# Performance work log

Hardware: AMD Instinct MI355X
Metric: run time of the kernel (lower is better)

Reference implementation:

```python
import jax, jax.numpy as jnp
import numpy as np

HIDDEN = 256
B, SQ, SKV = 8, 2048, 2048
SCALE = float(np.sqrt(HIDDEN / 2.0))  # module uses sqrt(hidden_dim/2)


def setup_inputs() -> dict:
    key = jax.random.key(0)
    ks = jax.random.split(key, 9)
    s = 1.0 / np.sqrt(HIDDEN)
    return {
        "query": jax.random.normal(ks[0], (B, SQ, HIDDEN), jnp.float32),
        "key": jax.random.normal(ks[1], (B, SKV, HIDDEN), jnp.float32),
        "value": jax.random.normal(ks[2], (B, SKV, HIDDEN), jnp.float32),
        "Wq": jax.random.uniform(ks[3], (HIDDEN, HIDDEN), jnp.float32, -s, s),
        "bq": jax.random.uniform(ks[4], (HIDDEN,), jnp.float32, -s, s),
        "Wk": jax.random.uniform(ks[5], (HIDDEN, HIDDEN), jnp.float32, -s, s),
        "bk": jax.random.uniform(ks[6], (HIDDEN,), jnp.float32, -s, s),
        "Wv": jax.random.uniform(ks[7], (HIDDEN, HIDDEN), jnp.float32, -s, s),
        "bv": jax.random.uniform(ks[8], (HIDDEN,), jnp.float32, -s, s),
    }


def reference(query, key, value, Wq, bq, Wk, bk, Wv, bv):
    # Linear projections (torch Linear: x @ W.T + b)
    Q = jnp.einsum('bsd,ed->bse', query, Wq) + bq  # [B,SQ,H]
    K = jnp.einsum('bsd,ed->bse', key, Wk) + bk    # [B,SKV,H]
    V = jnp.einsum('bsd,ed->bse', value, Wv) + bv  # [B,SKV,H]
    scores = jnp.einsum('bqd,bkd->bqk', Q, K) / SCALE  # [B,SQ,SKV]
    weights = jax.nn.softmax(scores, axis=-1)
    return jnp.einsum('bqk,bkd->bqd', weights, V)  # [B,SQ,H]
```

## Files before the change

kernel.cpp:

```cpp
#include <hip/hip_runtime.h>

#define HID 256
#define NB 8
#define SQL 2048
#define SKV 2048
#define SPLIT 4
#define KPB (SKV / SPLIT)
#define KVB 32
#define NT (KPB / KVB)
#define NROW (NB * SQL)

typedef __attribute__((ext_vector_type(8))) short bf16x8;
typedef __attribute__((ext_vector_type(4))) float f32x4;

static __device__ __forceinline__ unsigned short f2bf(float x) {
  union { float f; unsigned int u; } v; v.f = x;
  unsigned int r = v.u + 0x7FFFu + ((v.u >> 16) & 1u);
  return (unsigned short)(r >> 16);
}

__global__ void wconv_kernel(const float* __restrict__ Wq, const float* __restrict__ Wk,
                             const float* __restrict__ Wv, unsigned short* __restrict__ out) {
  int i = blockIdx.x * blockDim.x + threadIdx.x;
  if (i >= 3 * HID * HID) return;
  const float* src = (i < HID * HID) ? Wq : (i < 2 * HID * HID ? Wk : Wv);
  out[i] = f2bf(src[i & (HID * HID - 1)]);
}

__global__ __launch_bounds__(512, 4) void proj_kernel(
    const float* __restrict__ query, const float* __restrict__ key, const float* __restrict__ value,
    const unsigned short* __restrict__ Wb,
    const float* __restrict__ bq, const float* __restrict__ bk, const float* __restrict__ bv,
    unsigned short* __restrict__ Qb, unsigned short* __restrict__ KFo, unsigned short* __restrict__ VFo) {
  __shared__ __align__(16) char wl[65536];
  int tid = threadIdx.x;
  int wave = tid >> 6, lane = tid & 63, lr = lane & 15, lg = lane >> 4;
  int blk = blockIdx.x;
  int mat = blk >> 8;
  int rem = blk & 255;
  int b = rem >> 5;
  int rt = (rem >> 1) & 15;
  int et = rem & 1;

  const float* X = (mat == 0) ? query : (mat == 1 ? key : value);
  const float* bias = (mat == 0) ? bq : (mat == 1 ? bk : bv);
  const char* Wsrc = (const char*)(Wb + mat * HID * HID + et * 128 * HID);

#pragma unroll
  for (int i = 0; i < 8; i++) {
    int c = i * 512 + tid;
    int e = c >> 5;
    int glo = e * 512 + (((c & 31) ^ (e & 7)) << 4);
    __builtin_amdgcn_global_load_lds(
        (const __attribute__((address_space(1))) unsigned int*)(Wsrc + glo),
        (__attribute__((address_space(3))) unsigned int*)(wl + c * 16), 16, 0, 0);
  }

  int row_a = rt * 128 + wave * 16 + lr;
  const float* xrow = X + ((size_t)(b * SQL + row_a)) * HID;
  bf16x8 af[8];
#pragma unroll
  for (int s = 0; s < 8; s++) {
    const float4* p = (const float4*)(xrow + s * 32 + lg * 8);
    float4 x0 = p[0], x1 = p[1];
    bf16x8 a;
    a[0] = (short)f2bf(x0.x); a[1] = (short)f2bf(x0.y); a[2] = (short)f2bf(x0.z); a[3] = (short)f2bf(x0.w);
    a[4] = (short)f2bf(x1.x); a[5] = (short)f2bf(x1.y); a[6] = (short)f2bf(x1.z); a[7] = (short)f2bf(x1.w);
    af[s] = a;
  }
  __syncthreads();

  int row_c = rt * 128 + wave * 16 + lg * 4;
#pragma unroll
  for (int eo = 0; eo < 8; eo++) {
    f32x4 acc = (f32x4){0.f, 0.f, 0.f, 0.f};
    int eL = eo * 16 + lr;
#pragma unroll
    for (int sl = 0; sl < 8; sl++) {
      bf16x8 bfr = *(const bf16x8*)(wl + eL * 512 + (((sl * 4 + lg) ^ (eL & 7)) << 4));
      acc = __builtin_amdgcn_mfma_f32_16x16x32_bf16(af[sl], bfr, acc, 0, 0, 0);
    }
    int e = et * 128 + eo * 16 + lr;
    float bv_ = bias[e];
    if (mat == 0) {
      unsigned short* dst = Qb + (size_t)(b * SQL) * HID;
#pragma unroll
      for (int i = 0; i < 4; i++)
        dst[(size_t)(row_c + i) * HID + e] = f2bf(acc[i] + bv_);
    } else if (mat == 1) {
      int s = e >> 5, gg = (e >> 3) & 3, j = e & 7;
#pragma unroll
      for (int i = 0; i < 4; i++) {
        int row = row_c + i;
        int k5 = row & 31;
        int half = (k5 >> 2) & 1;
        int lidx = (((k5 >> 3) << 2) | (k5 & 3)) + 16 * gg;
        size_t frag = (size_t)(b * 1024 + (row >> 5) * 16 + half * 8 + s);
        KFo[frag * 512 + lidx * 8 + j] = f2bf(acc[i] + bv_);
      }
    } else {
      int dt = e >> 4, l15 = e & 15;
#pragma unroll
      for (int i = 0; i < 4; i++) {
        int row = row_c + i;
        int gg = (row >> 3) & 3, j = row & 7;
        size_t frag = (size_t)(b * 1024 + (row >> 5) * 16 + dt);
        VFo[frag * 512 + (l15 + 16 * gg) * 8 + j] = f2bf(acc[i] + bv_);
      }
    }
  }
}

__global__ __launch_bounds__(256, 2) void attn_kernel(
    const unsigned short* __restrict__ Qb, const char* __restrict__ KF,
    const char* __restrict__ VF, unsigned short* __restrict__ Op,
    float* __restrict__ Ml) {
  extern __shared__ char smem[];
  int tid = threadIdx.x;
  int wave = tid >> 6, lane = tid & 63, l15 = lane & 15, g = lane >> 4;
  int L = (blockIdx.x & 7) * 64 + (blockIdx.x >> 3);
  int b = L >> 6, sp = (L >> 4) & 3, qt = L & 15;
  int q0 = qt * 128 + wave * 32;

  const char* Ks0 = KF + ((size_t)(b * 64 + sp * 16)) * 16384;
  const char* Vs0 = VF + ((size_t)(b * 64 + sp * 16)) * 16384;

  auto stage = [&](int t, char* kb, char* vb) {
    const char* Ks = Ks0 + (size_t)t * 16384;
    const char* Vs = Vs0 + (size_t)t * 16384;
#pragma unroll
    for (int i = 0; i < 4; i++)
      __builtin_amdgcn_global_load_lds(
          (const __attribute__((address_space(1))) unsigned int*)(Ks + i * 4096 + tid * 16),
          (__attribute__((address_space(3))) unsigned int*)(kb + i * 4096 + tid * 16),
          16, 0, 0);
#pragma unroll
    for (int i = 0; i < 4; i++)
      __builtin_amdgcn_global_load_lds(
          (const __attribute__((address_space(1))) unsigned int*)(Vs + i * 4096 + tid * 16),
          (__attribute__((address_space(3))) unsigned int*)(vb + i * 4096 + tid * 16),
          16, 0, 0);
  };

  bf16x8 qfa[8], qfb[8];
  {
    const unsigned short* qa = Qb + ((size_t)(b * SQL + q0 + l15)) * HID + g * 8;
    const unsigned short* qb2 = qa + 16 * HID;
#pragma unroll
    for (int s = 0; s < 8; s++) {
      qfa[s] = *(const bf16x8*)(qa + s * 32);
      qfb[s] = *(const bf16x8*)(qb2 + s * 32);
    }
  }

  f32x4 acc0[16], acc1[16];
#pragma unroll
  for (int dt = 0; dt < 16; dt++) {
    acc0[dt] = (f32x4){0.f, 0.f, 0.f, 0.f};
    acc1[dt] = (f32x4){0.f, 0.f, 0.f, 0.f};
  }
  float m0 = -1e30f, l0 = 0.f, m1 = -1e30f, l1 = 0.f;
  const float kC = 1.44269504088896341f / 11.3137084989847604f;

  auto step = [&](const char* kb, const char* vb) {
    const char* kbl = kb + lane * 16;
    const char* vbl = vb + lane * 16;
    f32x4 p0a = (f32x4){0.f,0.f,0.f,0.f}, p1a = (f32x4){0.f,0.f,0.f,0.f};
    f32x4 p0b = (f32x4){0.f,0.f,0.f,0.f}, p1b = (f32x4){0.f,0.f,0.f,0.f};
#pragma unroll
    for (int s = 0; s < 8; s++) {
      bf16x8 kf0 = *(const bf16x8*)(kbl + s * 1024);
      bf16x8 kf1 = *(const bf16x8*)(kbl + (8 + s) * 1024);
      p0a = __builtin_amdgcn_mfma_f32_16x16x32_bf16(kf0, qfa[s], p0a, 0, 0, 0);
      p1a = __builtin_amdgcn_mfma_f32_16x16x32_bf16(kf1, qfa[s], p1a, 0, 0, 0);
      p0b = __builtin_amdgcn_mfma_f32_16x16x32_bf16(kf0, qfb[s], p0b, 0, 0, 0);
      p1b = __builtin_amdgcn_mfma_f32_16x16x32_bf16(kf1, qfb[s], p1b, 0, 0, 0);
    }

    float ta = fmaxf(fmaxf(fmaxf(p0a[0], p0a[1]), fmaxf(p0a[2], p0a[3])),
                     fmaxf(fmaxf(p1a[0], p1a[1]), fmaxf(p1a[2], p1a[3])));
    float tb = fmaxf(fmaxf(fmaxf(p0b[0], p0b[1]), fmaxf(p0b[2], p0b[3])),
                     fmaxf(fmaxf(p1b[0], p1b[1]), fmaxf(p1b[2], p1b[3])));
    ta = fmaxf(ta, __shfl_xor(ta, 16, 64)); tb = fmaxf(tb, __shfl_xor(tb, 16, 64));
    ta = fmaxf(ta, __shfl_xor(ta, 32, 64)); tb = fmaxf(tb, __shfl_xor(tb, 32, 64));
    float msa = ta * kC, msb = tb * kC;
    if (!__all(msa <= m0 + 8.0f)) {
      float mn = fmaxf(m0, msa);
      float al = exp2f(m0 - mn);
      l0 *= al; m0 = mn;
#pragma unroll
      for (int dt = 0; dt < 16; dt++)
#pragma unroll
        for (int i = 0; i < 4; i++) acc0[dt][i] *= al;
    }
    if (!__all(msb <= m1 + 8.0f)) {
      float mn = fmaxf(m1, msb);
      float al = exp2f(m1 - mn);
      l1 *= al; m1 = mn;
#pragma unroll
      for (int dt = 0; dt < 16; dt++)
#pragma unroll
        for (int i = 0; i < 4; i++) acc1[dt][i] *= al;
    }
#pragma unroll
    for (int i = 0; i < 4; i++) {
      p0a[i] = exp2f(fmaf(p0a[i], kC, -m0)); p1a[i] = exp2f(fmaf(p1a[i], kC, -m0));
      p0b[i] = exp2f(fmaf(p0b[i], kC, -m1)); p1b[i] = exp2f(fmaf(p1b[i], kC, -m1));
    }
    float sa = (p0a[0] + p0a[1]) + (p0a[2] + p0a[3]) + (p1a[0] + p1a[1]) + (p1a[2] + p1a[3]);
    float sb = (p0b[0] + p0b[1]) + (p0b[2] + p0b[3]) + (p1b[0] + p1b[1]) + (p1b[2] + p1b[3]);
    sa += __shfl_xor(sa, 16, 64); sb += __shfl_xor(sb, 16, 64);
    sa += __shfl_xor(sa, 32, 64); sb += __shfl_xor(sb, 32, 64);
    l0 += sa; l1 += sb;

    unsigned wa0, wa1, wa2, wa3, wb0, wb1, wb2, wb3;
    asm("v_cvt_pk_bf16_f32 %0, %1, %2" : "=v"(wa0) : "v"(p0a[0]), "v"(p0a[1]));
    asm("v_cvt_pk_bf16_f32 %0, %1, %2" : "=v"(wa1) : "v"(p0a[2]), "v"(p0a[3]));
    asm("v_cvt_pk_bf16_f32 %0, %1, %2" : "=v"(wa2) : "v"(p1a[0]), "v"(p1a[1]));
    asm("v_cvt_pk_bf16_f32 %0, %1, %2" : "=v"(wa3) : "v"(p1a[2]), "v"(p1a[3]));
    asm("v_cvt_pk_bf16_f32 %0, %1, %2" : "=v"(wb0) : "v"(p0b[0]), "v"(p0b[1]));
    asm("v_cvt_pk_bf16_f32 %0, %1, %2" : "=v"(wb1) : "v"(p0b[2]), "v"(p0b[3]));
    asm("v_cvt_pk_bf16_f32 %0, %1, %2" : "=v"(wb2) : "v"(p1b[0]), "v"(p1b[1]));
    asm("v_cvt_pk_bf16_f32 %0, %1, %2" : "=v"(wb3) : "v"(p1b[2]), "v"(p1b[3]));
    union { unsigned u[4]; bf16x8 v; } pa, pb;
    pa.u[0] = wa0; pa.u[1] = wa1; pa.u[2] = wa2; pa.u[3] = wa3;
    pb.u[0] = wb0; pb.u[1] = wb1; pb.u[2] = wb2; pb.u[3] = wb3;

#pragma unroll
    for (int dt = 0; dt < 16; dt++) {
      bf16x8 vf = *(const bf16x8*)(vbl + dt * 1024);
      acc0[dt] = __builtin_amdgcn_mfma_f32_16x16x32_bf16(vf, pa.v, acc0[dt], 0, 0, 0);
      acc1[dt] = __builtin_amdgcn_mfma_f32_16x16x32_bf16(vf, pb.v, acc1[dt], 0, 0, 0);
    }
  };

  stage(0, smem, smem + 32768);
  __syncthreads();
  for (int t = 0; t < NT; t++) {
    char* kb = smem + (t & 1) * 16384;
    char* vb = smem + 32768 + (t & 1) * 16384;
    if (t + 1 < NT)
      stage(t + 1, smem + ((t + 1) & 1) * 16384, smem + 32768 + ((t + 1) & 1) * 16384);
    step(kb, vb);
    __syncthreads();
  }

  size_t rowA = (size_t)b * SQL + q0 + l15;
  size_t rowB = rowA + 16;
  if (g == 0) {
    float2 mlA; mlA.x = m0; mlA.y = l0;
    float2 mlB; mlB.x = m1; mlB.y = l1;
    *(float2*)(Ml + ((size_t)sp * NROW + rowA) * 2) = mlA;
    *(float2*)(Ml + ((size_t)sp * NROW + rowB) * 2) = mlB;
  }
  float li0 = 1.0f / l0, li1 = 1.0f / l1;
  unsigned short* oA = Op + ((size_t)sp * NROW + rowA) * HID;
  unsigned short* oB = Op + ((size_t)sp * NROW + rowB) * HID;
#pragma unroll
  for (int dt = 0; dt < 16; dt++) {
    ushort4 v0, v1;
    union { _Float16 hf; unsigned short u; } c;
    c.hf = (_Float16)(acc0[dt][0] * li0); v0.x = c.u;
    c.hf = (_Float16)(acc0[dt][1] * li0); v0.y = c.u;
    c.hf = (_Float16)(acc0[dt][2] * li0); v0.z = c.u;
    c.hf = (_Float16)(acc0[dt][3] * li0); v0.w = c.u;
    c.hf = (_Float16)(acc1[dt][0] * li1); v1.x = c.u;
    c.hf = (_Float16)(acc1[dt][1] * li1); v1.y = c.u;
    c.hf = (_Float16)(acc1[dt][2] * li1); v1.z = c.u;
    c.hf = (_Float16)(acc1[dt][3] * li1); v1.w = c.u;
    *(ushort4*)(oA + dt * 16 + g * 4) = v0;
    *(ushort4*)(oB + dt * 16 + g * 4) = v1;
  }
}

__global__ __launch_bounds__(256) void comb_kernel(const unsigned short* __restrict__ Op,
                                                   const float* __restrict__ Ml,
                                                   float* __restrict__ out) {
  int idx = blockIdx.x * 256 + threadIdx.x;
  int row = idx >> 6;
  int d0 = (idx & 63) << 2;
  float mv[SPLIT], lv[SPLIT];
#pragma unroll
  for (int s = 0; s < SPLIT; s++) {
    float2 ml = *(const float2*)(Ml + ((size_t)s * NROW + row) * 2);
    mv[s] = ml.x; lv[s] = ml.y;
  }
  float M = mv[0];
#pragma unroll
  for (int s = 1; s < SPLIT; s++) M = fmaxf(M, mv[s]);
  float W = 0.f, w[SPLIT];
#pragma unroll
  for (int s = 0; s < SPLIT; s++) { w[s] = lv[s] * exp2f(mv[s] - M); W += w[s]; }
  float wi = 1.0f / W;
  float o0 = 0.f, o1 = 0.f, o2 = 0.f, o3 = 0.f;
#pragma unroll
  for (int s = 0; s < SPLIT; s++) {
    ushort4 u = *(const ushort4*)(Op + ((size_t)s * NROW + row) * HID + d0);
    union { unsigned short us; _Float16 hf; } c0, c1, c2, c3;
    c0.us = u.x; c1.us = u.y; c2.us = u.z; c3.us = u.w;
    o0 += w[s] * (float)c0.hf; o1 += w[s] * (float)c1.hf;
    o2 += w[s] * (float)c2.hf; o3 += w[s] * (float)c3.hf;
  }
  float4 res; res.x = o0 * wi; res.y = o1 * wi; res.z = o2 * wi; res.w = o3 * wi;
  *(float4*)(out + (size_t)row * HID + d0) = res;
}

extern "C" void kernel_launch(void* const* d_in, const int* in_sizes, int n_in,
                              void* d_out, int out_size, void* d_ws, size_t ws_size,
                              hipStream_t stream) {
  const float* query = (const float*)d_in[0];
  const float* key   = (const float*)d_in[1];
  const float* value = (const float*)d_in[2];
  const float* Wq = (const float*)d_in[3];
  const float* bq = (const float*)d_in[4];
  const float* Wk = (const float*)d_in[5];
  const float* bk = (const float*)d_in[6];
  const float* Wv = (const float*)d_in[7];
  const float* bv = (const float*)d_in[8];

  char* ws = (char*)d_ws;
  unsigned short* Wb  = (unsigned short*)ws;
  unsigned short* Qb  = (unsigned short*)(ws + 393216);
  unsigned short* KF  = Qb + (size_t)NB * SQL * HID;
  unsigned short* VF  = KF + (size_t)NB * SKV * HID;
  unsigned short* Op  = VF + (size_t)NB * HID * SKV;
  float* Ml = (float*)(Op + (size_t)SPLIT * NROW * HID);

  hipLaunchKernelGGL(wconv_kernel, dim3(768), dim3(256), 0, stream, Wq, Wk, Wv, Wb);
  hipLaunchKernelGGL(proj_kernel, dim3(768), dim3(512), 0, stream,
                     query, key, value, Wb, bq, bk, bv, Qb, KF, VF);
  hipLaunchKernelGGL(attn_kernel, dim3(512), dim3(256), 65536, stream,
                     Qb, (const char*)KF, (const char*)VF, Op, Ml);
  hipLaunchKernelGGL(comb_kernel, dim3(4096), dim3(256), 0, stream, Op, Ml, (float*)d_out);
}
```

Baseline: 92.24 us.

## Reuse input fragments across both output halves and add separate K fragment transpose kernel

The projection kernel now covers both 128-column halves of the output in one block, loading each weight half into LDS in turn. This halves the grid and avoids converting the same input rows to bf16 twice. K is written row-major into scratch space that aliases the partial-output buffer, then reordered into the fragment layout by a new small transpose kernel, which replaces scattered 2-byte stores with 16-byte copies. V stores become packed ushort4 writes. In attention, the per-tile cross-lane shuffle reduction of the row sum is moved to after the loop, at the cost of one extra kernel launch and an extra round trip of K through memory.

```diff
diff --git a/kernel.cpp b/kernel.cpp
--- a/kernel.cpp
+++ b/kernel.cpp
@@ -27,34 +27,22 @@
   out[i] = f2bf(src[i & (HID * HID - 1)]);
 }
 
-__global__ __launch_bounds__(512, 4) void proj_kernel(
+__global__ __launch_bounds__(512, 2) void proj_kernel(
     const float* __restrict__ query, const float* __restrict__ key, const float* __restrict__ value,
     const unsigned short* __restrict__ Wb,
     const float* __restrict__ bq, const float* __restrict__ bk, const float* __restrict__ bv,
-    unsigned short* __restrict__ Qb, unsigned short* __restrict__ KFo, unsigned short* __restrict__ VFo) {
+    unsigned short* __restrict__ Qb, unsigned short* __restrict__ Kr, unsigned short* __restrict__ VFo) {
   __shared__ __align__(16) char wl[65536];
   int tid = threadIdx.x;
   int wave = tid >> 6, lane = tid & 63, lr = lane & 15, lg = lane >> 4;
   int blk = blockIdx.x;
-  int mat = blk >> 8;
-  int rem = blk & 255;
-  int b = rem >> 5;
-  int rt = (rem >> 1) & 15;
-  int et = rem & 1;
+  int mat = blk >> 7;
+  int rem = blk & 127;
+  int b = rem >> 4;
+  int rt = rem & 15;
 
   const float* X = (mat == 0) ? query : (mat == 1 ? key : value);
   const float* bias = (mat == 0) ? bq : (mat == 1 ? bk : bv);
-  const char* Wsrc = (const char*)(Wb + mat * HID * HID + et * 128 * HID);
-
-#pragma unroll
-  for (int i = 0; i < 8; i++) {
-    int c = i * 512 + tid;
-    int e = c >> 5;
-    int glo = e * 512 + (((c & 31) ^ (e & 7)) << 4);
-    __builtin_amdgcn_global_load_lds(
-        (const __attribute__((address_space(1))) unsigned int*)(Wsrc + glo),
-        (__attribute__((address_space(3))) unsigned int*)(wl + c * 16), 16, 0, 0);
-  }
 
   int row_a = rt * 128 + wave * 16 + lr;
   const float* xrow = X + ((size_t)(b * SQL + row_a)) * HID;
@@ -68,47 +56,60 @@
     a[4] = (short)f2bf(x1.x); a[5] = (short)f2bf(x1.y); a[6] = (short)f2bf(x1.z); a[7] = (short)f2bf(x1.w);
     af[s] = a;
   }
-  __syncthreads();
 
   int row_c = rt * 128 + wave * 16 + lg * 4;
-#pragma unroll
-  for (int eo = 0; eo < 8; eo++) {
-    f32x4 acc = (f32x4){0.f, 0.f, 0.f, 0.f};
-    int eL = eo * 16 + lr;
-#pragma unroll
-    for (int sl = 0; sl < 8; sl++) {
-      bf16x8 bfr = *(const bf16x8*)(wl + eL * 512 + (((sl * 4 + lg) ^ (eL & 7)) << 4));
-      acc = __builtin_amdgcn_mfma_f32_16x16x32_bf16(af[sl], bfr, acc, 0, 0, 0);
-    }
-    int e = et * 128 + eo * 16 + lr;
-    float bv_ = bias[e];
-    if (mat == 0) {
-      unsigned short* dst = Qb + (size_t)(b * SQL) * HID;
-#pragma unroll
-      for (int i = 0; i < 4; i++)
-        dst[(size_t)(row_c + i) * HID + e] = f2bf(acc[i] + bv_);
-    } else if (mat == 1) {
-      int s = e >> 5, gg = (e >> 3) & 3, j = e & 7;
-#pragma unroll
-      for (int i = 0; i < 4; i++) {
-        int row = row_c + i;
-        int k5 = row & 31;
-        int half = (k5 >> 2) & 1;
-        int lidx = (((k5 >> 3) << 2) | (k5 & 3)) + 16 * gg;
-        size_t frag = (size_t)(b * 1024 + (row >> 5) * 16 + half * 8 + s);
-        KFo[frag * 512 + lidx * 8 + j] = f2bf(acc[i] + bv_);
+  for (int et = 0; et < 2; ++et) {
+    if (et) __syncthreads();
+    const char* Wsrc = (const char*)(Wb + mat * HID * HID + et * 128 * HID);
+#pragma unroll
+    for (int i = 0; i < 8; i++) {
+      int c = i * 512 + tid;
+      int e = c >> 5;
+      int glo = e * 512 + (((c & 31) ^ (e & 7)) << 4);
+      __builtin_amdgcn_global_load_lds(
+          (const __attribute__((address_space(1))) unsigned int*)(Wsrc + glo),
+          (__attribute__((address_space(3))) unsigned int*)(wl + c * 16), 16, 0, 0);
+    }
+    __syncthreads();
+
+#pragma unroll
+    for (int eo = 0; eo < 8; eo++) {
+      f32x4 acc = (f32x4){0.f, 0.f, 0.f, 0.f};
+      int eL = eo * 16 + lr;
+#pragma unroll
+      for (int sl = 0; sl < 8; sl++) {
+        bf16x8 bfr = *(const bf16x8*)(wl + eL * 512 + (((sl * 4 + lg) ^ (eL & 7)) << 4));
+        acc = __builtin_amdgcn_mfma_f32_16x16x32_bf16(af[sl], bfr, acc, 0, 0, 0);
       }
-    } else {
-      int dt = e >> 4, l15 = e & 15;
-#pragma unroll
-      for (int i = 0; i < 4; i++) {
-        int row = row_c + i;
-        int gg = (row >> 3) & 3, j = row & 7;
-        size_t frag = (size_t)(b * 1024 + (row >> 5) * 16 + dt);
-        VFo[frag * 512 + (l15 + 16 * gg) * 8 + j] = f2bf(acc[i] + bv_);
+      int e = et * 128 + eo * 16 + lr;
+      float bv_ = bias[e];
+      if (mat < 2) {
+        unsigned short* dst = (mat == 0 ? Qb : Kr) + (size_t)(b * SQL) * HID;
+#pragma unroll
+        for (int i = 0; i < 4; i++)
+          dst[(size_t)(row_c + i) * HID + e] = f2bf(acc[i] + bv_);
+      } else {
+        int jb = 4 * ((row_c >> 4) & 1);
+        size_t frag = (size_t)b * 1024 + (size_t)(row_c >> 5) * 16 + (et * 8 + eo);
+        ushort4 v;
+        v.x = f2bf(acc[0] + bv_); v.y = f2bf(acc[1] + bv_);
+        v.z = f2bf(acc[2] + bv_); v.w = f2bf(acc[3] + bv_);
+        *(ushort4*)(VFo + frag * 512 + (lr + 16 * lg) * 8 + jb) = v;
       }
     }
   }
+}
+
+__global__ __launch_bounds__(256) void ktr_kernel(const unsigned short* __restrict__ Kr,
+                                                  unsigned short* __restrict__ KFo) {
+  int o = blockIdx.x * 256 + threadIdx.x;
+  int cidx = o & 63, frag = o >> 6;
+  int b = frag >> 10, r = frag & 1023;
+  int tile = r >> 4, half = (r >> 3) & 1, s = r & 7;
+  int l15 = cidx & 15, g = cidx >> 4;
+  int ky = tile * 32 + half * 16 + l15;
+  *(float4*)(KFo + (size_t)frag * 512 + cidx * 8) =
+      *(const float4*)(Kr + ((size_t)b * SKV + ky) * HID + s * 32 + g * 8);
 }
 
 __global__ __launch_bounds__(256, 2) void attn_kernel(
@@ -207,11 +208,8 @@
       p0a[i] = exp2f(fmaf(p0a[i], kC, -m0)); p1a[i] = exp2f(fmaf(p1a[i], kC, -m0));
       p0b[i] = exp2f(fmaf(p0b[i], kC, -m1)); p1b[i] = exp2f(fmaf(p1b[i], kC, -m1));
     }
-    float sa = (p0a[0] + p0a[1]) + (p0a[2] + p0a[3]) + (p1a[0] + p1a[1]) + (p1a[2] + p1a[3]);
-    float sb = (p0b[0] + p0b[1]) + (p0b[2] + p0b[3]) + (p1b[0] + p1b[1]) + (p1b[2] + p1b[3]);
-    sa += __shfl_xor(sa, 16, 64); sb += __shfl_xor(sb, 16, 64);
-    sa += __shfl_xor(sa, 32, 64); sb += __shfl_xor(sb, 32, 64);
-    l0 += sa; l1 += sb;
+    l0 += (p0a[0] + p0a[1]) + (p0a[2] + p0a[3]) + (p1a[0] + p1a[1]) + (p1a[2] + p1a[3]);
+    l1 += (p0b[0] + p0b[1]) + (p0b[2] + p0b[3]) + (p1b[0] + p1b[1]) + (p1b[2] + p1b[3]);
 
     unsigned wa0, wa1, wa2, wa3, wb0, wb1, wb2, wb3;
     asm("v_cvt_pk_bf16_f32 %0, %1, %2" : "=v"(wa0) : "v"(p0a[0]), "v"(p0a[1]));
@@ -244,6 +242,9 @@
     step(kb, vb);
     __syncthreads();
   }
+
+  l0 += __shfl_xor(l0, 16, 64); l0 += __shfl_xor(l0, 32, 64);
+  l1 += __shfl_xor(l1, 16, 64); l1 += __shfl_xor(l1, 32, 64);
 
   size_t rowA = (size_t)b * SQL + q0 + l15;
   size_t rowB = rowA + 16;
@@ -325,10 +326,12 @@
   unsigned short* VF  = KF + (size_t)NB * SKV * HID;
   unsigned short* Op  = VF + (size_t)NB * HID * SKV;
   float* Ml = (float*)(Op + (size_t)SPLIT * NROW * HID);
+  unsigned short* Kr = Op;
 
   hipLaunchKernelGGL(wconv_kernel, dim3(768), dim3(256), 0, stream, Wq, Wk, Wv, Wb);
-  hipLaunchKernelGGL(proj_kernel, dim3(768), dim3(512), 0, stream,
-                     query, key, value, Wb, bq, bk, bv, Qb, KF, VF);
+  hipLaunchKernelGGL(proj_kernel, dim3(384), dim3(512), 0, stream,
+                     query, key, value, Wb, bq, bk, bv, Qb, Kr, VF);
+  hipLaunchKernelGGL(ktr_kernel, dim3(2048), dim3(256), 0, stream, Kr, KF);
   hipLaunchKernelGGL(attn_kernel, dim3(512), dim3(256), 65536, stream,
                      Qb, (const char*)KF, (const char*)VF, Op, Ml);
   hipLaunchKernelGGL(comb_kernel, dim3(4096), dim3(256), 0, stream, Op, Ml, (float*)d_out);
```

Measured after the change: 91.49 us. No clear change (-0.8%).
